# Optimization experiments

Hardware: AMD Instinct MI355X
Metric: run time of the kernel (lower is better)

## Reference

```python
import jax, jax.numpy as jnp
import numpy as np

NUM_HEADS = 32
HEAD_DIM = 128
NUM_KV_HEADS = 8
Q_LEN = 1024
MAX_SEQ = 4096
CACHE_BATCH = 4
SEQ_POS = 1024
BATCH_POS = 1


def setup_inputs() -> dict:
    key = jax.random.key(0)
    ks = jax.random.split(key, 6)
    query_state = jax.random.normal(ks[0], (1, NUM_HEADS, Q_LEN, HEAD_DIM), jnp.float32)
    key_state = jax.random.normal(ks[1], (1, NUM_KV_HEADS, Q_LEN, HEAD_DIM), jnp.float32)
    value_state = jax.random.normal(ks[2], (1, NUM_KV_HEADS, Q_LEN, HEAD_DIM), jnp.float32)
    past_key_state = jax.random.normal(ks[3], (CACHE_BATCH, NUM_KV_HEADS, MAX_SEQ, HEAD_DIM), jnp.float32)
    past_value_state = jax.random.normal(ks[4], (CACHE_BATCH, NUM_KV_HEADS, MAX_SEQ, HEAD_DIM), jnp.float32)
    # Causal prefill mask: query token i (global pos SEQ_POS+i) may attend to cache pos m <= SEQ_POS+i
    i = jnp.arange(Q_LEN)[:, None] + SEQ_POS
    j = jnp.arange(MAX_SEQ)[None, :]
    attn_mask = (j <= i).astype(jnp.float32)[None, None]  # [1,1,Q_LEN,MAX_SEQ]
    scale = jnp.array([1.0 / np.sqrt(HEAD_DIM)], jnp.float32)
    return {
        "query_state": query_state,
        "key_state": key_state,
        "value_state": value_state,
        "attn_mask": attn_mask,
        "batch_position": BATCH_POS,
        "past_key_state": past_key_state,
        "past_value_state": past_value_state,
        "seq_position": SEQ_POS,
        "scale": scale,
    }


def reference(query_state, key_state, value_state, attn_mask, batch_position,
              past_key_state, past_value_state, seq_position, scale):
    g = NUM_HEADS // NUM_KV_HEADS
    q_len = query_state.shape[2]
    # --- cache update (prefill: insert new K/V at [batch_position, :, seq_position:seq_position+q_len]) ---
    k_cache = jax.lax.dynamic_update_slice(past_key_state, key_state, (batch_position, 0, seq_position, 0))
    v_cache = jax.lax.dynamic_update_slice(past_value_state, value_state, (batch_position, 0, seq_position, 0))
    # --- grouped-query attention over the updated cache row ---
    q = query_state.reshape(1, NUM_KV_HEADS, g, q_len, HEAD_DIM)
    k = jax.lax.dynamic_slice_in_dim(k_cache, batch_position, 1, axis=0)[0]  # [kvh, MAX_SEQ, hd]
    v = jax.lax.dynamic_slice_in_dim(v_cache, batch_position, 1, axis=0)[0]
    scores = jnp.einsum('bkgqd,kmd->bkgqm', q, k) * scale[0]  # [1,kvh,g,q,MAX_SEQ]
    neg = jnp.finfo(scores.dtype).min
    scores = jnp.where(attn_mask[:, :, None] > 0.5, scores, neg)
    probs = jax.nn.softmax(scores, axis=-1)
    out = jnp.einsum('bkgqm,kmd->bkgqd', probs, v)  # [1,kvh,g,q,hd]
    out = out.reshape(1, NUM_HEADS, q_len, HEAD_DIM)
    attn_output = out.transpose(0, 2, 1, 3).reshape(1, q_len, NUM_HEADS * HEAD_DIM)
    return attn_output, k_cache, v_cache
```

## Files before the change

kernel.cpp:

```cpp
#include <hip/hip_runtime.h>

#define NH 32
#define KVHN 8
#define HD 128
#define QL 1024
#define MS 4096
#define KVB 64

typedef __bf16 bf16x8 __attribute__((ext_vector_type(8)));
typedef __bf16 bf16x4 __attribute__((ext_vector_type(4)));
typedef float f32x4 __attribute__((ext_vector_type(4)));
typedef float f32x16 __attribute__((ext_vector_type(16)));


__device__ __forceinline__ void gload16(const void* g, void* l) {
    __builtin_amdgcn_global_load_lds(
        (const __attribute__((address_space(1))) unsigned int*)g,
        (__attribute__((address_space(3))) unsigned int*)l, 16, 0, 0);
}

__device__ __forceinline__ unsigned int pk2(float a, float b) {
    union { __bf16 h; unsigned short u; } x, y;
    x.h = (__bf16)a; y.h = (__bf16)b;
    return (unsigned int)x.u | ((unsigned int)y.u << 16);
}

__device__ __forceinline__ float exp2fast(float x) {
    return __builtin_amdgcn_exp2f(x);
}

__global__ __launch_bounds__(256) void cache_update_kernel(
    const float4* __restrict__ kn, const float4* __restrict__ vn,
    const float4* __restrict__ pk, const float4* __restrict__ pv,
    const int* __restrict__ bp_p, const int* __restrict__ sp_p,
    float4* __restrict__ ok, float4* __restrict__ ov,
    __bf16* __restrict__ kbf, __bf16* __restrict__ vt)
{
    __shared__ float vtile[8][132];
    int i = blockIdx.x * 256 + threadIdx.x;
    int bp = *bp_p, sp = *sp_p;
    int d4  = i & 31;
    int pos = (i >> 5) & 4095;
    int kvh = (i >> 17) & 7;
    int b   = i >> 20;
    float4 kv4, vv4;
    if (b == bp && pos >= sp && pos < sp + QL) {
        int ns = (kvh * QL + (pos - sp)) * 32 + d4;
        kv4 = kn[ns]; vv4 = vn[ns];
    } else {
        kv4 = pk[i]; vv4 = pv[i];
    }
    ok[i] = kv4; ov[i] = vv4;
    if (b == bp) {
        bf16x4 o;
        o[0] = (__bf16)kv4.x; o[1] = (__bf16)kv4.y;
        o[2] = (__bf16)kv4.z; o[3] = (__bf16)kv4.w;
        int c16 = d4 >> 1, half = d4 & 1;
        *(bf16x4*)(kbf + ((size_t)kvh * MS + pos) * HD
                       + ((c16 ^ (pos & 7)) * 8 + half * 4)) = o;
        *(float4*)&vtile[threadIdx.x >> 5][d4 * 4] = vv4;
    }
    __syncthreads();
    if (b == bp && threadIdx.x < 128) {
        int d  = threadIdx.x;
        int p0 = (blockIdx.x * 8) & 4095;
        int pt = p0 >> 6, chk = (p0 & 63) >> 3;
        bf16x8 o;
        #pragma unroll
        for (int j = 0; j < 8; ++j) o[j] = (__bf16)vtile[j][d];
        *(bf16x8*)(vt + (((size_t)kvh * 64 + pt) * HD + d) * 64
                      + ((chk ^ (d & 7)) * 8)) = o;
    }
}

__global__ __launch_bounds__(256, 2) void attn_kernel(
    const float* __restrict__ q,
    const int* __restrict__ sp_p,
    const float* __restrict__ scale_p,
    const __bf16* __restrict__ kbf, const __bf16* __restrict__ vt,
    float* __restrict__ out)
{
    __shared__ __align__(16) unsigned char smem[65536];

    const int sp = *sp_p;
    const float scl = *scale_p * 1.44269504088896340736f;

    int bid = blockIdx.x;
    int kvh = bid & 7;
    int inner = (bid & 255) >> 3;
    int headLocal = inner & 3;
    int j = inner >> 2;
    int qtile = (bid < 256) ? j : 15 - j;
    int head = kvh * 4 + headLocal;

    const int q0     = qtile * 64;
    const int tid    = threadIdx.x;
    const int wave   = tid >> 6;
    const int qsub   = wave & 1;
    const int kvhalf = wave >> 1;
    const int lane   = tid & 63;
    const int hi     = lane >> 5;
    const int c31    = lane & 31;
    const int qb     = q0 + qsub * 32;
    const int myq    = qb + c31;

    const unsigned char* krow = (const unsigned char*)(kbf + (size_t)kvh * MS * HD);
    const unsigned char* vrow = (const unsigned char*)(vt + (size_t)kvh * 64 * HD * 64);

    bf16x8 qf[8];
    #pragma unroll
    for (int dc = 0; dc < 8; ++dc) {
        const float* src = q + ((size_t)(head * QL + qb + c31) * HD + dc * 16 + hi * 8);
        float4 f0 = *(const float4*)src;
        float4 f1 = *(const float4*)(src + 4);
        bf16x8 v;
        v[0]=(__bf16)(f0.x*scl); v[1]=(__bf16)(f0.y*scl);
        v[2]=(__bf16)(f0.z*scl); v[3]=(__bf16)(f0.w*scl);
        v[4]=(__bf16)(f1.x*scl); v[5]=(__bf16)(f1.y*scl);
        v[6]=(__bf16)(f1.z*scl); v[7]=(__bf16)(f1.w*scl);
        qf[dc] = v;
    }

    f32x16 acc[4];
    #pragma unroll
    for (int dsub = 0; dsub < 4; ++dsub)
        #pragma unroll
        for (int r = 0; r < 16; ++r) acc[dsub][r] = 0.f;
    float m_run = -1e30f, l_run = 0.f;

    const int n_super = (sp + q0 + 64) >> 6;

    auto stage = [&](int buf, int t) {
        const unsigned char* kt = krow + (size_t)t * 16384;
        const unsigned char* vtile = vrow + (size_t)t * 16384;
        unsigned char* kl = smem + buf * 32768;
        unsigned char* vl = kl + 16384;
        #pragma unroll
        for (int p = 0; p < 4; ++p) {
            int off = p * 4096 + tid * 16;
            gload16(kt + off, kl + off);
            gload16(vtile + off, vl + off);
        }
    };

    int cur = 0;
    stage(0, 0);
    __syncthreads();

    for (int it = 0; it < n_super; ++it) {
        const int n0 = it * KVB + kvhalf * 32;
        if (it + 1 < n_super) stage(cur ^ 1, it + 1);

        const unsigned char* Ksm = smem + cur * 32768;
        const unsigned char* Vsm = Ksm + 16384;

        f32x16 st0, st1;
        #pragma unroll
        for (int r = 0; r < 16; ++r) { st0[r] = 0.f; st1[r] = 0.f; }
        int kr = kvhalf * 32 + c31;
        __builtin_amdgcn_s_setprio(1);
        #pragma unroll
        for (int dc = 0; dc < 4; ++dc) {
            bf16x8 ka = *(const bf16x8*)(Ksm + kr * 256 + (((2 * dc + hi) ^ (kr & 7)) << 4));
            st0 = __builtin_amdgcn_mfma_f32_32x32x16_bf16(ka, qf[dc], st0, 0, 0, 0);
            bf16x8 kb = *(const bf16x8*)(Ksm + kr * 256 + (((2 * (dc + 4) + hi) ^ (kr & 7)) << 4));
            st1 = __builtin_amdgcn_mfma_f32_32x32x16_bf16(kb, qf[dc + 4], st1, 0, 0, 0);
        }
        __builtin_amdgcn_s_setprio(0);
        f32x16 st = st0 + st1;

        const bool need_mask = (n0 + 31) > (sp + qb);
        if (need_mask) {
            #pragma unroll
            for (int r = 0; r < 16; ++r) {
                int kvg = n0 + (r & 3) + 8 * (r >> 2) + 4 * hi;
                if (kvg > sp + myq) st[r] = -1e30f;
            }
        }
        float m01 = fmaxf(fmaxf(st[0], st[1]), fmaxf(st[2], st[3]));
        float m23 = fmaxf(fmaxf(st[4], st[5]), fmaxf(st[6], st[7]));
        float m45 = fmaxf(fmaxf(st[8], st[9]), fmaxf(st[10], st[11]));
        float m67 = fmaxf(fmaxf(st[12], st[13]), fmaxf(st[14], st[15]));
        float mx = fmaxf(fmaxf(m01, m23), fmaxf(m45, m67));
        mx = fmaxf(mx, __shfl_xor(mx, 32));

        if (!__all(mx <= m_run + 8.0f)) {
            float nm = fmaxf(m_run, mx);
            float corr = exp2fast(m_run - nm);
            m_run = nm;
            l_run *= corr;
            #pragma unroll
            for (int r = 0; r < 16; ++r) {
                int qsrc = (r & 3) + 8 * (r >> 2) + 4 * hi;
                float cq = __shfl(corr, qsrc);
                acc[0][r] *= cq; acc[1][r] *= cq; acc[2][r] *= cq; acc[3][r] *= cq;
            }
        }

        #pragma unroll
        for (int r = 0; r < 16; ++r) st[r] = exp2fast(st[r] - m_run);
        {
            float s0 = (st[0] + st[1]) + (st[2] + st[3]);
            float s1 = (st[4] + st[5]) + (st[6] + st[7]);
            float s2 = (st[8] + st[9]) + (st[10] + st[11]);
            float s3 = (st[12] + st[13]) + (st[14] + st[15]);
            l_run += (s0 + s1) + (s2 + s3);
        }

        unsigned int loW[4], hiW[4];
        #pragma unroll
        for (int qd = 0; qd < 2; ++qd) {
            int b = qd * 8;
            loW[qd*2+0] = pk2(st[b+0], st[b+1]);
            loW[qd*2+1] = pk2(st[b+2], st[b+3]);
            hiW[qd*2+0] = pk2(st[b+4], st[b+5]);
            hiW[qd*2+1] = pk2(st[b+6], st[b+7]);
        }
        bf16x8 pfrag[2];
        #pragma unroll
        for (int qd = 0; qd < 2; ++qd) {
            unsigned int a0 = loW[qd*2+0], b0 = hiW[qd*2+0];
            unsigned int a1 = loW[qd*2+1], b1 = hiW[qd*2+1];
            asm("v_permlane32_swap_b32 %0, %1" : "+v"(a0), "+v"(b0));
            asm("v_permlane32_swap_b32 %0, %1" : "+v"(a1), "+v"(b1));
            union { unsigned int u[4]; bf16x8 v; } fu;
            fu.u[0] = a0; fu.u[1] = a1; fu.u[2] = b0; fu.u[3] = b1;
            pfrag[qd] = fu.v;
        }

        __builtin_amdgcn_s_setprio(1);
        #pragma unroll
        for (int dsub = 0; dsub < 4; ++dsub) {
            int vr = dsub * 32 + c31;
            #pragma unroll
            for (int qd = 0; qd < 2; ++qd) {
                int ksg = kvhalf * 2 + qd;
                bf16x8 vf = *(const bf16x8*)(Vsm + vr * 128 + (((ksg * 2 + hi) ^ (vr & 7)) << 4));
                acc[dsub] = __builtin_amdgcn_mfma_f32_32x32x16_bf16(pfrag[qd], vf, acc[dsub], 0, 0, 0);
            }
        }
        __builtin_amdgcn_s_setprio(0);

        __syncthreads();
        cur ^= 1;
    }

    float l_full = l_run + __shfl_xor(l_run, 32);
    float* mlm = (float*)smem;
    float* mll = (float*)smem + 128;
    if (hi == 0) { mlm[wave * 32 + c31] = m_run; mll[wave * 32 + c31] = l_full; }
    __syncthreads();
    int pw = wave ^ 2;
    float m_o = mlm[pw * 32 + c31];
    float l_o = mll[pw * 32 + c31];
    float m_n = fmaxf(m_run, m_o);
    float sc   = exp2fast(m_run - m_n);
    float sc_o = exp2fast(m_o - m_n);
    float linv = 1.0f / (l_full * sc + l_o * sc_o);
    float* Oex = (float*)(smem + 1024) + (size_t)qsub * 32 * 128;
    if (kvhalf) {
        #pragma unroll
        for (int r = 0; r < 16; ++r) {
            int qsrc = (r & 3) + 8 * (r >> 2) + 4 * hi;
            float s = __shfl(sc, qsrc);
            #pragma unroll
            for (int dsub = 0; dsub < 4; ++dsub)
                Oex[qsrc * 128 + dsub * 32 + c31] = acc[dsub][r] * s;
        }
    }
    __syncthreads();
    if (!kvhalf) {
        #pragma unroll
        for (int r = 0; r < 16; ++r) {
            int qsrc = (r & 3) + 8 * (r >> 2) + 4 * hi;
            float s  = __shfl(sc, qsrc);
            float lq = __shfl(linv, qsrc);
            float* orow = out + (size_t)(qb + qsrc) * (NH * HD) + head * HD;
            #pragma unroll
            for (int dsub = 0; dsub < 4; ++dsub)
                orow[dsub * 32 + c31] =
                    (acc[dsub][r] * s + Oex[qsrc * 128 + dsub * 32 + c31]) * lq;
        }
    }
}

extern "C" void kernel_launch(void* const* d_in, const int* in_sizes, int n_in,
                              void* d_out, int out_size, void* d_ws, size_t ws_size,
                              hipStream_t stream)
{
    const float* q_st   = (const float*)d_in[0];
    const float* k_new  = (const float*)d_in[1];
    const float* v_new  = (const float*)d_in[2];
    const int*   bp_p   = (const int*)d_in[4];
    const float* past_k = (const float*)d_in[5];
    const float* past_v = (const float*)d_in[6];
    const int*   sp_p   = (const int*)d_in[7];
    const float* scl_p  = (const float*)d_in[8];

    float* out_attn = (float*)d_out;
    float* out_k    = out_attn + (size_t)QL * NH * HD;
    float* out_v    = out_k + (size_t)4 * KVHN * MS * HD;

    __bf16* kbf = (__bf16*)d_ws;
    __bf16* vtw = kbf + (size_t)KVHN * MS * HD;

    cache_update_kernel<<<16384, 256, 0, stream>>>(
        (const float4*)k_new, (const float4*)v_new,
        (const float4*)past_k, (const float4*)past_v,
        bp_p, sp_p, (float4*)out_k, (float4*)out_v, kbf, vtw);

    attn_kernel<<<512, 256, 0, stream>>>(
        q_st, sp_p, scl_p, kbf, vtw, out_attn);
}
```

Baseline: 106.3 us.

## Overlap full KV cache copy with attention compute inside attention kernel

The first kernel now only packs the active batch row into bf16 K and transposed V, and no longer copies the whole fp32 cache. The full cache copy for both K and V is spread across the 512 attention blocks. Each block copies 16 chunks, interleaved with its QK^T MFMA loop, so the memory-bound copy can hide behind compute. Blocks with fewer KV iterations finish their chunks after the loop. This adds register pressure and global traffic inside the attention kernel, which may disturb its pipelining.

```diff
diff --git a/kernel.cpp b/kernel.cpp
--- a/kernel.cpp
+++ b/kernel.cpp
@@ -29,29 +29,27 @@
     return __builtin_amdgcn_exp2f(x);
 }
 
-__global__ __launch_bounds__(256) void cache_update_kernel(
+__global__ __launch_bounds__(256) void pack_kernel(
     const float4* __restrict__ kn, const float4* __restrict__ vn,
     const float4* __restrict__ pk, const float4* __restrict__ pv,
     const int* __restrict__ bp_p, const int* __restrict__ sp_p,
-    float4* __restrict__ ok, float4* __restrict__ ov,
     __bf16* __restrict__ kbf, __bf16* __restrict__ vt)
 {
     __shared__ float vtile[8][132];
-    int i = blockIdx.x * 256 + threadIdx.x;
+    int li = blockIdx.x * 256 + threadIdx.x;
     int bp = *bp_p, sp = *sp_p;
-    int d4  = i & 31;
-    int pos = (i >> 5) & 4095;
-    int kvh = (i >> 17) & 7;
-    int b   = i >> 20;
+    int d4  = li & 31;
+    int pos = (li >> 5) & 4095;
+    int kvh = li >> 17;
     float4 kv4, vv4;
-    if (b == bp && pos >= sp && pos < sp + QL) {
+    if (pos >= sp && pos < sp + QL) {
         int ns = (kvh * QL + (pos - sp)) * 32 + d4;
         kv4 = kn[ns]; vv4 = vn[ns];
     } else {
-        kv4 = pk[i]; vv4 = pv[i];
-    }
-    ok[i] = kv4; ov[i] = vv4;
-    if (b == bp) {
+        int gi = (bp << 20) + li;
+        kv4 = pk[gi]; vv4 = pv[gi];
+    }
+    {
         bf16x4 o;
         o[0] = (__bf16)kv4.x; o[1] = (__bf16)kv4.y;
         o[2] = (__bf16)kv4.z; o[3] = (__bf16)kv4.w;
@@ -61,7 +59,7 @@
         *(float4*)&vtile[threadIdx.x >> 5][d4 * 4] = vv4;
     }
     __syncthreads();
-    if (b == bp && threadIdx.x < 128) {
+    if (threadIdx.x < 128) {
         int d  = threadIdx.x;
         int p0 = (blockIdx.x * 8) & 4095;
         int pt = p0 >> 6, chk = (p0 & 63) >> 3;
@@ -75,14 +73,18 @@
 
 __global__ __launch_bounds__(256, 2) void attn_kernel(
     const float* __restrict__ q,
-    const int* __restrict__ sp_p,
+    const int* __restrict__ bp_p, const int* __restrict__ sp_p,
     const float* __restrict__ scale_p,
     const __bf16* __restrict__ kbf, const __bf16* __restrict__ vt,
+    const float4* __restrict__ knf, const float4* __restrict__ vnf,
+    const float4* __restrict__ pkf, const float4* __restrict__ pvf,
+    float4* __restrict__ okf, float4* __restrict__ ovf,
     float* __restrict__ out)
 {
     __shared__ __align__(16) unsigned char smem[65536];
 
     const int sp = *sp_p;
+    const int bp = *bp_p;
     const float scl = *scale_p * 1.44269504088896340736f;
 
     int bid = blockIdx.x;
@@ -92,6 +94,11 @@
     int j = inner >> 2;
     int qtile = (bid < 256) ? j : 15 - j;
     int head = kvh * 4 + headLocal;
+
+    const float4* csrc_new  = (bid < 256) ? knf : vnf;
+    const float4* csrc_past = (bid < 256) ? pkf : pvf;
+    float4*       cdst      = (bid < 256) ? okf : ovf;
+    const int     cbase     = (bid & 255) * 16384;
 
     const int q0     = qtile * 64;
     const int tid    = threadIdx.x;
@@ -143,6 +150,25 @@
         }
     };
 
+    auto copy_load = [&](int slot, float4* cbuf) {
+        #pragma unroll
+        for (int jj = 0; jj < 4; ++jj) {
+            int idx = cbase + slot * 1024 + jj * 256 + tid;
+            int d4  = idx & 31;
+            int pos = (idx >> 5) & 4095;
+            int ck  = (idx >> 17) & 7;
+            int b   = idx >> 20;
+            cbuf[jj] = (b == bp && pos >= sp && pos < sp + QL)
+                ? csrc_new[(ck * QL + (pos - sp)) * 32 + d4]
+                : csrc_past[idx];
+        }
+    };
+    auto copy_store = [&](int slot, const float4* cbuf) {
+        #pragma unroll
+        for (int jj = 0; jj < 4; ++jj)
+            cdst[cbase + slot * 1024 + jj * 256 + tid] = cbuf[jj];
+    };
+
     int cur = 0;
     stage(0, 0);
     __syncthreads();
@@ -150,6 +176,10 @@
     for (int it = 0; it < n_super; ++it) {
         const int n0 = it * KVB + kvhalf * 32;
         if (it + 1 < n_super) stage(cur ^ 1, it + 1);
+
+        float4 cbuf[4];
+        const bool do_copy = (it < 16);
+        if (do_copy) copy_load(it, cbuf);
 
         const unsigned char* Ksm = smem + cur * 32768;
         const unsigned char* Vsm = Ksm + 16384;
@@ -168,6 +198,8 @@
         }
         __builtin_amdgcn_s_setprio(0);
         f32x16 st = st0 + st1;
+
+        if (do_copy) copy_store(it, cbuf);
 
         const bool need_mask = (n0 + 31) > (sp + qb);
         if (need_mask) {
@@ -243,6 +275,12 @@
 
         __syncthreads();
         cur ^= 1;
+    }
+
+    for (int ct = (n_super < 16 ? n_super : 16); ct < 16; ++ct) {
+        float4 cbuf[4];
+        copy_load(ct, cbuf);
+        copy_store(ct, cbuf);
     }
 
     float l_full = l_run + __shfl_xor(l_run, 32);
@@ -304,11 +342,14 @@
     __bf16* kbf = (__bf16*)d_ws;
     __bf16* vtw = kbf + (size_t)KVHN * MS * HD;
 
-    cache_update_kernel<<<16384, 256, 0, stream>>>(
+    pack_kernel<<<4096, 256, 0, stream>>>(
         (const float4*)k_new, (const float4*)v_new,
         (const float4*)past_k, (const float4*)past_v,
-        bp_p, sp_p, (float4*)out_k, (float4*)out_v, kbf, vtw);
+        bp_p, sp_p, kbf, vtw);
 
     attn_kernel<<<512, 256, 0, stream>>>(
-        q_st, sp_p, scl_p, kbf, vtw, out_attn);
-}
+        q_st, bp_p, sp_p, scl_p, kbf, vtw,
+        (const float4*)k_new, (const float4*)v_new,
+        (const float4*)past_k, (const float4*)past_v,
+        (float4*)out_k, (float4*)out_v, out_attn);
+}
```

After: 133.7 us. 25.8% more time.
